# Kernel tuning notes

Hardware: AMD Instinct MI355X
Metric: run time of the kernel (lower is better)

Reference implementation:

```python
import jax, jax.numpy as jnp
import numpy as np

SEQ_LEN = 4096
D_IN = 1024
D_OUT = 1024


def setup_inputs() -> dict:
    key = jax.random.key(0)
    k_x, k_q, k_k, k_v = jax.random.split(key, 4)
    s = 1.0 / np.sqrt(D_IN)
    return {
        "x": jax.random.normal(k_x, (SEQ_LEN, D_IN), dtype=jnp.float32),
        "W_query": jax.random.normal(k_q, (D_IN, D_OUT), dtype=jnp.float32) * s,
        "W_key": jax.random.normal(k_k, (D_IN, D_OUT), dtype=jnp.float32) * s,
        "W_value": jax.random.normal(k_v, (D_IN, D_OUT), dtype=jnp.float32) * s,
    }


def reference(x, W_query, W_key, W_value):
    # QKV projections (Linear without bias): [S, d_out]
    q = x @ W_query
    k = x @ W_key
    v = x @ W_value
    # Full S x S score matrix, causal mask, scaled softmax
    scores = q @ k.T  # [S, S]
    seq_len = x.shape[0]
    causal = jnp.tril(jnp.ones((seq_len, seq_len), dtype=bool))
    scores = jnp.where(causal, scores, -jnp.inf)
    scale = 1.0 / jnp.sqrt(jnp.asarray(k.shape[-1], dtype=scores.dtype))
    attn = jax.nn.softmax(scores * scale, axis=-1)
    return attn @ v  # [S, d_out]
```

## Files before the change

### kernel.cpp

```cpp
#include <hip/hip_runtime.h>
#include <math.h>

#define SEQ 4096
#define DIM 1024

typedef unsigned short u16;
typedef __attribute__((ext_vector_type(8))) short short8;
typedef __attribute__((ext_vector_type(4))) float floatx4;
typedef __attribute__((ext_vector_type(4))) unsigned short us4;

__device__ __forceinline__ float bf2f(u16 u) {
    union { unsigned int i; float f; } c; c.i = ((unsigned int)u) << 16; return c.f;
}
__device__ __forceinline__ u16 f2bf(float f) {
    union { float f; unsigned int i; } c; c.f = f;
    return (u16)((c.i + 0x7fffu + ((c.i >> 16) & 1u)) >> 16);
}
__device__ __forceinline__ void gload_lds16(const u16* g, u16* l) {
    __builtin_amdgcn_global_load_lds((const __attribute__((address_space(1))) void*)g,
                                     (__attribute__((address_space(3))) void*)l, 16, 0, 0);
}

__global__ __launch_bounds__(256) void gemm_qkv(const u16* __restrict__ A,
                                                const u16* __restrict__ B,
                                                u16* __restrict__ QK,
                                                u16* __restrict__ VtOut) {
    const int row0 = blockIdx.x * 128;
    const int col0 = blockIdx.y * 128;

    __shared__ u16 As[3][4096];
    __shared__ u16 Bs[3][4096];

    const int tid  = threadIdx.x;
    const int wave = tid >> 6;
    const int lane = tid & 63;
    const int wm = wave & 1;
    const int wn = wave >> 1;

    const int s0 = wave * 128 + lane;
    const int s1 = s0 + 64;
    const int r0s = s0 >> 2, q0s = ((s0 & 3) ^ ((s0 >> 3) & 3)) * 8;
    const int r1s = s1 >> 2, q1s = ((s1 & 3) ^ ((s1 >> 3) & 3)) * 8;
    const u16* aP0 = A + (size_t)(row0 + r0s) * DIM + q0s;
    const u16* aP1 = A + (size_t)(row0 + r1s) * DIM + q1s;
    const u16* bP0 = B + (size_t)(col0 + r0s) * DIM + q0s;
    const u16* bP1 = B + (size_t)(col0 + r1s) * DIM + q1s;
    const int l0 = wave * 1024;

    floatx4 acc[4][4] = {};
    const int niter = DIM >> 5;
    const int frow = lane & 15;
    const int xq = (((lane >> 4) ^ ((frow >> 1) & 3))) * 8;

    gload_lds16(aP0, &As[0][l0]);
    gload_lds16(aP1, &As[0][l0 + 512]);
    gload_lds16(bP0, &Bs[0][l0]);
    gload_lds16(bP1, &Bs[0][l0 + 512]);
    aP0 += 32; aP1 += 32; bP0 += 32; bP1 += 32;
    gload_lds16(aP0, &As[1][l0]);
    gload_lds16(aP1, &As[1][l0 + 512]);
    gload_lds16(bP0, &Bs[1][l0]);
    gload_lds16(bP1, &Bs[1][l0 + 512]);
    aP0 += 32; aP1 += 32; bP0 += 32; bP1 += 32;

    auto compute_tile = [&](int c) {
        short8 af[4], bfr[4];
#pragma unroll
        for (int t = 0; t < 4; ++t) {
            af[t]  = *(const short8*)&As[c][(wm * 64 + t * 16 + frow) * 32 + xq];
            bfr[t] = *(const short8*)&Bs[c][(wn * 64 + t * 16 + frow) * 32 + xq];
        }
#pragma unroll
        for (int mt = 0; mt < 4; ++mt)
#pragma unroll
            for (int nt = 0; nt < 4; ++nt)
                acc[mt][nt] = __builtin_amdgcn_mfma_f32_16x16x32_bf16(
                    af[mt], bfr[nt], acc[mt][nt], 0, 0, 0);
    };

    int cur = 0, pre = 2;
    for (int it = 0; it < niter - 2; ++it) {
        asm volatile("s_waitcnt vmcnt(4)\n\ts_barrier" ::: "memory");
        short8 af[4], bfr[4];
#pragma unroll
        for (int t = 0; t < 4; ++t) {
            af[t]  = *(const short8*)&As[cur][(wm * 64 + t * 16 + frow) * 32 + xq];
            bfr[t] = *(const short8*)&Bs[cur][(wn * 64 + t * 16 + frow) * 32 + xq];
        }
        gload_lds16(aP0, &As[pre][l0]);
        gload_lds16(aP1, &As[pre][l0 + 512]);
        gload_lds16(bP0, &Bs[pre][l0]);
        gload_lds16(bP1, &Bs[pre][l0 + 512]);
        aP0 += 32; aP1 += 32; bP0 += 32; bP1 += 32;
#pragma unroll
        for (int mt = 0; mt < 4; ++mt)
#pragma unroll
            for (int nt = 0; nt < 4; ++nt)
                acc[mt][nt] = __builtin_amdgcn_mfma_f32_16x16x32_bf16(
                    af[mt], bfr[nt], acc[mt][nt], 0, 0, 0);
        cur = (cur == 2) ? 0 : cur + 1;
        pre = (pre == 2) ? 0 : pre + 1;
    }
    asm volatile("s_waitcnt vmcnt(4)\n\ts_barrier" ::: "memory");
    compute_tile(cur);
    cur = (cur == 2) ? 0 : cur + 1;
    asm volatile("s_waitcnt vmcnt(0)\n\ts_barrier" ::: "memory");
    compute_tile(cur);

    const int cr = (lane >> 4) * 4;
    const int cc = lane & 15;
    if (col0 >= 2048) {
#pragma unroll
        for (int mt = 0; mt < 4; ++mt)
#pragma unroll
            for (int nt = 0; nt < 4; ++nt) {
                const int row = row0 + wm * 64 + mt * 16 + cr;
                const int col = (col0 - 2048) + wn * 64 + nt * 16 + cc;
                us4 o = { f2bf(acc[mt][nt][0]), f2bf(acc[mt][nt][1]),
                          f2bf(acc[mt][nt][2]), f2bf(acc[mt][nt][3]) };
                *(us4*)&VtOut[(size_t)col * SEQ + row] = o;
            }
    } else {
        const float sc = (col0 < 1024) ? 0.03125f : 1.0f;
#pragma unroll
        for (int mt = 0; mt < 4; ++mt)
#pragma unroll
            for (int nt = 0; nt < 4; ++nt)
#pragma unroll
                for (int r = 0; r < 4; ++r) {
                    const int row = row0 + wm * 64 + mt * 16 + cr + r;
                    const int col = col0 + wn * 64 + nt * 16 + cc;
                    QK[(size_t)row * 2048 + col] = f2bf(acc[mt][nt][r] * sc);
                }
    }
}

template <int SCORES>
__global__ __launch_bounds__(512, 4) void gemm_att(const u16* __restrict__ A,
                                                   const u16* __restrict__ B,
                                                   void* __restrict__ Cv,
                                                   float* __restrict__ Lsum,
                                                   int lda, int ldb) {
    int row0, col0, kbeg = 0, kend;
    if (SCORES) {
        col0 = blockIdx.x * 128;
        row0 = blockIdx.y * 128;
        if (col0 > row0) return;
        kend = DIM;
    } else {
        const int u = blockIdx.x;
        col0 = blockIdx.y * 128;
        int r, c;
        if (u < 32)      { c = 0; r = u; }
        else if (u < 56) { c = 1; r = u - 24; }
        else if (u < 72) { c = 2; r = u - 40; }
        else             { c = 3; r = u - 48; }
        row0 = r * 128;
        kbeg = c << 10;
        kend = min(kbeg + 1024, row0 + 128);
    }

    __shared__ u16 As[3][4096];
    __shared__ u16 Bs[3][4096];

    const int tid  = threadIdx.x;
    const int wave = tid >> 6;
    const int lane = tid & 63;
    const int wm = wave & 1;
    const int wn = wave >> 1;

    const int sw = wave & 3;
    const int s0 = sw * 128 + lane;
    const int s1 = s0 + 64;
    const int r0s = s0 >> 2, q0s = ((s0 & 3) ^ ((s0 >> 3) & 3)) * 8;
    const int r1s = s1 >> 2, q1s = ((s1 & 3) ^ ((s1 >> 3) & 3)) * 8;
    const bool isA = wave < 4;
    const u16* p0 = isA ? A + (size_t)(row0 + r0s) * lda + kbeg + q0s
                        : B + (size_t)(col0 + r0s) * ldb + kbeg + q0s;
    const u16* p1 = isA ? A + (size_t)(row0 + r1s) * lda + kbeg + q1s
                        : B + (size_t)(col0 + r1s) * ldb + kbeg + q1s;
    const int o0 = s0 * 8;
    const int o1 = o0 + 512;

    floatx4 acc[4][2] = {};
    const int niter = (kend - kbeg) >> 5;
    const int frow = lane & 15;
    const int xq = (((lane >> 4) ^ ((frow >> 1) & 3))) * 8;

    {
        u16* d0 = isA ? &As[0][0] : &Bs[0][0];
        gload_lds16(p0, d0 + o0);
        gload_lds16(p1, d0 + o1);
        p0 += 32; p1 += 32;
        u16* d1 = isA ? &As[1][0] : &Bs[1][0];
        gload_lds16(p0, d1 + o0);
        gload_lds16(p1, d1 + o1);
        p0 += 32; p1 += 32;
    }

    auto compute_tile = [&](int c) {
        short8 af[4], bfr[2];
#pragma unroll
        for (int t = 0; t < 4; ++t)
            af[t] = *(const short8*)&As[c][(wm * 64 + t * 16 + frow) * 32 + xq];
#pragma unroll
        for (int t = 0; t < 2; ++t)
            bfr[t] = *(const short8*)&Bs[c][(wn * 32 + t * 16 + frow) * 32 + xq];
#pragma unroll
        for (int mt = 0; mt < 4; ++mt)
#pragma unroll
            for (int nt = 0; nt < 2; ++nt)
                acc[mt][nt] = __builtin_amdgcn_mfma_f32_16x16x32_bf16(
                    af[mt], bfr[nt], acc[mt][nt], 0, 0, 0);
    };

    int cur = 0, pre = 2;
    for (int it = 0; it < niter - 2; ++it) {
        asm volatile("s_waitcnt vmcnt(2)\n\ts_barrier" ::: "memory");
        short8 af[4], bfr[2];
#pragma unroll
        for (int t = 0; t < 4; ++t)
            af[t] = *(const short8*)&As[cur][(wm * 64 + t * 16 + frow) * 32 + xq];
#pragma unroll
        for (int t = 0; t < 2; ++t)
            bfr[t] = *(const short8*)&Bs[cur][(wn * 32 + t * 16 + frow) * 32 + xq];
        u16* dp = isA ? &As[pre][0] : &Bs[pre][0];
        gload_lds16(p0, dp + o0);
        gload_lds16(p1, dp + o1);
        p0 += 32; p1 += 32;
#pragma unroll
        for (int mt = 0; mt < 4; ++mt)
#pragma unroll
            for (int nt = 0; nt < 2; ++nt)
                acc[mt][nt] = __builtin_amdgcn_mfma_f32_16x16x32_bf16(
                    af[mt], bfr[nt], acc[mt][nt], 0, 0, 0);
        cur = (cur == 2) ? 0 : cur + 1;
        pre = (pre == 2) ? 0 : pre + 1;
    }
    asm volatile("s_waitcnt vmcnt(2)\n\ts_barrier" ::: "memory");
    compute_tile(cur);
    cur = (cur == 2) ? 0 : cur + 1;
    asm volatile("s_waitcnt vmcnt(0)\n\ts_barrier" ::: "memory");
    compute_tile(cur);

    const int cr = (lane >> 4) * 4;
    const int cc = lane & 15;
    if (SCORES) {
        u16* E = (u16*)Cv;
#pragma unroll
        for (int mt = 0; mt < 4; ++mt) {
#pragma unroll
            for (int r = 0; r < 4; ++r) {
                const int grow = row0 + wm * 64 + mt * 16 + cr + r;
                float rowsum = 0.f;
#pragma unroll
                for (int nt = 0; nt < 2; ++nt) {
                    const int gcol = col0 + wn * 32 + nt * 16 + cc;
                    const float e = (gcol <= grow) ? __expf(acc[mt][nt][r]) : 0.f;
                    rowsum += e;
                    E[(size_t)grow * SEQ + gcol] = f2bf(e);
                }
                rowsum += __shfl_xor(rowsum, 1);
                rowsum += __shfl_xor(rowsum, 2);
                rowsum += __shfl_xor(rowsum, 4);
                rowsum += __shfl_xor(rowsum, 8);
                if (cc == 0) atomicAdd(&Lsum[grow], rowsum);
            }
        }
    } else {
        float* O = (float*)Cv;
#pragma unroll
        for (int mt = 0; mt < 4; ++mt)
#pragma unroll
            for (int r = 0; r < 4; ++r) {
                const int grow = row0 + wm * 64 + mt * 16 + cr + r;
                const float invl = 1.0f / Lsum[grow];
#pragma unroll
                for (int nt = 0; nt < 2; ++nt) {
                    const int col = col0 + wn * 32 + nt * 16 + cc;
                    atomicAdd(&O[(size_t)grow * DIM + col], acc[mt][nt][r] * invl);
                }
            }
    }
}

__global__ __launch_bounds__(256) void prep(const float* __restrict__ x,
                                            const float* __restrict__ W0,
                                            const float* __restrict__ W1,
                                            const float* __restrict__ W2,
                                            u16* __restrict__ xb,
                                            u16* __restrict__ Wt,
                                            float* __restrict__ O,
                                            float* __restrict__ Lsum) {
    __shared__ float tile[32][33];
    const int b = blockIdx.x;
    const int tid = threadIdx.x;
    if (b < 4096) {
        const size_t i = ((size_t)b * 256 + tid) * 4;
        const float4 v = *(const float4*)(x + i);
        us4 o = { f2bf(v.x), f2bf(v.y), f2bf(v.z), f2bf(v.w) };
        *(us4*)(xb + i) = o;
    } else if (b < 7168) {
        const int t = b - 4096;
        const int z = t >> 10;
        const int idx = t & 1023;
        const float* W = (z == 0) ? W0 : (z == 1) ? W1 : W2;
        u16* out = Wt + (size_t)z * DIM * DIM;
        const int bx = (idx & 31) * 32;
        const int by = (idx >> 5) * 32;
        const int tx = tid & 31;
        const int ty = (tid >> 5) * 4;
#pragma unroll
        for (int r = 0; r < 4; ++r)
            tile[ty + r][tx] = W[(size_t)(by + ty + r) * DIM + bx + tx];
        __syncthreads();
#pragma unroll
        for (int r = 0; r < 4; ++r)
            out[(size_t)(bx + ty + r) * DIM + by + tx] = f2bf(tile[tx][ty + r]);
    } else {
        const int t = b - 7168;
        const size_t i = ((size_t)t * 256 + tid) * 4;
        *(float4*)(O + i) = make_float4(0.f, 0.f, 0.f, 0.f);
        if (t < 4) *(float4*)(Lsum + (size_t)(t * 256 + tid) * 4) =
            make_float4(0.f, 0.f, 0.f, 0.f);
    }
}

extern "C" void kernel_launch(void* const* d_in, const int* in_sizes, int n_in,
                              void* d_out, int out_size, void* d_ws, size_t ws_size,
                              hipStream_t stream) {
    const float* x  = (const float*)d_in[0];
    const float* Wq = (const float*)d_in[1];
    const float* Wk = (const float*)d_in[2];
    const float* Wv = (const float*)d_in[3];

    u16* xb   = (u16*)d_ws;
    u16* Wt   = xb + (size_t)SEQ * DIM;
    u16* QK   = Wt + (size_t)3072 * DIM;
    u16* Vt   = QK + (size_t)SEQ * 2048;
    u16* E    = Vt + (size_t)DIM * SEQ;
    float* Lsum = (float*)(E + (size_t)SEQ * SEQ);

    prep<<<8192, 256, 0, stream>>>(x, Wq, Wk, Wv, xb, Wt, (float*)d_out, Lsum);

    gemm_qkv<<<dim3(32, 24), 256, 0, stream>>>(xb, Wt, QK, Vt);

    gemm_att<1><<<dim3(32, 32), 512, 0, stream>>>(
        QK, QK + 1024, E, Lsum, 2048, 2048);

    gemm_att<0><<<dim3(80, 8), 512, 0, stream>>>(
        E, Vt, d_out, Lsum, SEQ, SEQ);
}
```

Before: 209.3 us.

## Restructure attention GEMMs to 4-wave blocks with 64-wide K tiles and triangular grid

The scores and PV kernels move from 512-thread blocks with a 32-wide K step and triple buffering to 256-thread blocks with a 64-wide K step and double buffering. Each wave now computes a 64x64 sub-tile with a 4x4 MFMA accumulator, which gives more data reuse per LDS read. The scores launch becomes a 1D triangular grid of 528 blocks, so no blocks are launched only to exit, and the PV grid swaps its x and y axes. The costs are a full vmcnt(0) wait every iteration, meaning less load/compute overlap, and more registers per wave.

```diff
diff --git a/kernel.cpp b/kernel.cpp
--- a/kernel.cpp
+++ b/kernel.cpp
@@ -136,20 +136,24 @@
 }
 
 template <int SCORES>
-__global__ __launch_bounds__(512, 4) void gemm_att(const u16* __restrict__ A,
-                                                   const u16* __restrict__ B,
-                                                   void* __restrict__ Cv,
-                                                   float* __restrict__ Lsum,
-                                                   int lda, int ldb) {
+__global__ __launch_bounds__(256) void gemm_att64(const u16* __restrict__ A,
+                                                  const u16* __restrict__ B,
+                                                  void* __restrict__ Cv,
+                                                  float* __restrict__ Lsum,
+                                                  int lda, int ldb) {
     int row0, col0, kbeg = 0, kend;
     if (SCORES) {
-        col0 = blockIdx.x * 128;
-        row0 = blockIdx.y * 128;
-        if (col0 > row0) return;
+        const int t = blockIdx.x;
+        int by = (int)((sqrtf(8.0f * t + 1.0f) - 1.0f) * 0.5f);
+        while ((by + 1) * (by + 2) / 2 <= t) ++by;
+        while (by * (by + 1) / 2 > t) --by;
+        const int bx = t - by * (by + 1) / 2;
+        row0 = by * 128;
+        col0 = bx * 128;
         kend = DIM;
     } else {
-        const int u = blockIdx.x;
-        col0 = blockIdx.y * 128;
+        col0 = blockIdx.x * 128;
+        const int u = blockIdx.y;
         int r, c;
         if (u < 32)      { c = 0; r = u; }
         else if (u < 56) { c = 1; r = u - 24; }
@@ -160,8 +164,8 @@
         kend = min(kbeg + 1024, row0 + 128);
     }
 
-    __shared__ u16 As[3][4096];
-    __shared__ u16 Bs[3][4096];
+    __shared__ u16 As[2][8192];
+    __shared__ u16 Bs[2][8192];
 
     const int tid  = threadIdx.x;
     const int wave = tid >> 6;
@@ -169,79 +173,64 @@
     const int wm = wave & 1;
     const int wn = wave >> 1;
 
-    const int sw = wave & 3;
-    const int s0 = sw * 128 + lane;
-    const int s1 = s0 + 64;
-    const int r0s = s0 >> 2, q0s = ((s0 & 3) ^ ((s0 >> 3) & 3)) * 8;
-    const int r1s = s1 >> 2, q1s = ((s1 & 3) ^ ((s1 >> 3) & 3)) * 8;
-    const bool isA = wave < 4;
-    const u16* p0 = isA ? A + (size_t)(row0 + r0s) * lda + kbeg + q0s
-                        : B + (size_t)(col0 + r0s) * ldb + kbeg + q0s;
-    const u16* p1 = isA ? A + (size_t)(row0 + r1s) * lda + kbeg + q1s
-                        : B + (size_t)(col0 + r1s) * ldb + kbeg + q1s;
-    const int o0 = s0 * 8;
-    const int o1 = o0 + 512;
-
-    floatx4 acc[4][2] = {};
-    const int niter = (kend - kbeg) >> 5;
+    const u16* aP[4];
+    const u16* bP[4];
+    int dOff[4];
+#pragma unroll
+    for (int j = 0; j < 4; ++j) {
+        const int s = wave * 256 + j * 64 + lane;
+        const int r = s >> 3;
+        const int q = (s & 7) ^ (r & 7);
+        aP[j] = A + (size_t)(row0 + r) * lda + kbeg + q * 8;
+        bP[j] = B + (size_t)(col0 + r) * ldb + kbeg + q * 8;
+        dOff[j] = s * 8;
+    }
+
+    floatx4 acc[4][4] = {};
+    const int niter = (kend - kbeg) >> 6;
     const int frow = lane & 15;
-    const int xq = (((lane >> 4) ^ ((frow >> 1) & 3))) * 8;
-
-    {
-        u16* d0 = isA ? &As[0][0] : &Bs[0][0];
-        gload_lds16(p0, d0 + o0);
-        gload_lds16(p1, d0 + o1);
-        p0 += 32; p1 += 32;
-        u16* d1 = isA ? &As[1][0] : &Bs[1][0];
-        gload_lds16(p0, d1 + o0);
-        gload_lds16(p1, d1 + o1);
-        p0 += 32; p1 += 32;
-    }
-
-    auto compute_tile = [&](int c) {
-        short8 af[4], bfr[2];
-#pragma unroll
-        for (int t = 0; t < 4; ++t)
-            af[t] = *(const short8*)&As[c][(wm * 64 + t * 16 + frow) * 32 + xq];
-#pragma unroll
-        for (int t = 0; t < 2; ++t)
-            bfr[t] = *(const short8*)&Bs[c][(wn * 32 + t * 16 + frow) * 32 + xq];
-#pragma unroll
-        for (int mt = 0; mt < 4; ++mt)
-#pragma unroll
-            for (int nt = 0; nt < 2; ++nt)
-                acc[mt][nt] = __builtin_amdgcn_mfma_f32_16x16x32_bf16(
-                    af[mt], bfr[nt], acc[mt][nt], 0, 0, 0);
-    };
-
-    int cur = 0, pre = 2;
-    for (int it = 0; it < niter - 2; ++it) {
-        asm volatile("s_waitcnt vmcnt(2)\n\ts_barrier" ::: "memory");
-        short8 af[4], bfr[2];
-#pragma unroll
-        for (int t = 0; t < 4; ++t)
-            af[t] = *(const short8*)&As[cur][(wm * 64 + t * 16 + frow) * 32 + xq];
-#pragma unroll
-        for (int t = 0; t < 2; ++t)
-            bfr[t] = *(const short8*)&Bs[cur][(wn * 32 + t * 16 + frow) * 32 + xq];
-        u16* dp = isA ? &As[pre][0] : &Bs[pre][0];
-        gload_lds16(p0, dp + o0);
-        gload_lds16(p1, dp + o1);
-        p0 += 32; p1 += 32;
-#pragma unroll
-        for (int mt = 0; mt < 4; ++mt)
-#pragma unroll
-            for (int nt = 0; nt < 2; ++nt)
-                acc[mt][nt] = __builtin_amdgcn_mfma_f32_16x16x32_bf16(
-                    af[mt], bfr[nt], acc[mt][nt], 0, 0, 0);
-        cur = (cur == 2) ? 0 : cur + 1;
-        pre = (pre == 2) ? 0 : pre + 1;
-    }
-    asm volatile("s_waitcnt vmcnt(2)\n\ts_barrier" ::: "memory");
-    compute_tile(cur);
-    cur = (cur == 2) ? 0 : cur + 1;
-    asm volatile("s_waitcnt vmcnt(0)\n\ts_barrier" ::: "memory");
-    compute_tile(cur);
+    const int grp  = lane >> 4;
+
+#pragma unroll
+    for (int j = 0; j < 4; ++j) {
+        gload_lds16(aP[j], &As[0][dOff[j]]);
+        gload_lds16(bP[j], &Bs[0][dOff[j]]);
+        aP[j] += 64; bP[j] += 64;
+    }
+
+    for (int it = 0; it < niter; ++it) {
+        asm volatile("s_waitcnt vmcnt(0)\n\ts_barrier" ::: "memory");
+        const int cur = it & 1;
+        short8 af[2][4], bfr[2][4];
+#pragma unroll
+        for (int ks = 0; ks < 2; ++ks)
+#pragma unroll
+            for (int t = 0; t < 4; ++t) {
+                const int ar = wm * 64 + t * 16 + frow;
+                const int ca = (ks * 4 + grp) ^ (ar & 7);
+                af[ks][t] = *(const short8*)&As[cur][ar * 64 + ca * 8];
+                const int br = wn * 64 + t * 16 + frow;
+                const int cb = (ks * 4 + grp) ^ (br & 7);
+                bfr[ks][t] = *(const short8*)&Bs[cur][br * 64 + cb * 8];
+            }
+        if (it + 1 < niter) {
+            const int nxt = cur ^ 1;
+#pragma unroll
+            for (int j = 0; j < 4; ++j) {
+                gload_lds16(aP[j], &As[nxt][dOff[j]]);
+                gload_lds16(bP[j], &Bs[nxt][dOff[j]]);
+                aP[j] += 64; bP[j] += 64;
+            }
+        }
+#pragma unroll
+        for (int ks = 0; ks < 2; ++ks)
+#pragma unroll
+            for (int mt = 0; mt < 4; ++mt)
+#pragma unroll
+                for (int nt = 0; nt < 4; ++nt)
+                    acc[mt][nt] = __builtin_amdgcn_mfma_f32_16x16x32_bf16(
+                        af[ks][mt], bfr[ks][nt], acc[mt][nt], 0, 0, 0);
+    }
 
     const int cr = (lane >> 4) * 4;
     const int cc = lane & 15;
@@ -254,8 +243,8 @@
                 const int grow = row0 + wm * 64 + mt * 16 + cr + r;
                 float rowsum = 0.f;
 #pragma unroll
-                for (int nt = 0; nt < 2; ++nt) {
-                    const int gcol = col0 + wn * 32 + nt * 16 + cc;
+                for (int nt = 0; nt < 4; ++nt) {
+                    const int gcol = col0 + wn * 64 + nt * 16 + cc;
                     const float e = (gcol <= grow) ? __expf(acc[mt][nt][r]) : 0.f;
                     rowsum += e;
                     E[(size_t)grow * SEQ + gcol] = f2bf(e);
@@ -276,8 +265,8 @@
                 const int grow = row0 + wm * 64 + mt * 16 + cr + r;
                 const float invl = 1.0f / Lsum[grow];
 #pragma unroll
-                for (int nt = 0; nt < 2; ++nt) {
-                    const int col = col0 + wn * 32 + nt * 16 + cc;
+                for (int nt = 0; nt < 4; ++nt) {
+                    const int col = col0 + wn * 64 + nt * 16 + cc;
                     atomicAdd(&O[(size_t)grow * DIM + col], acc[mt][nt][r] * invl);
                 }
             }
@@ -345,9 +334,7 @@
 
     gemm_qkv<<<dim3(32, 24), 256, 0, stream>>>(xb, Wt, QK, Vt);
 
-    gemm_att<1><<<dim3(32, 32), 512, 0, stream>>>(
-        QK, QK + 1024, E, Lsum, 2048, 2048);
-
-    gemm_att<0><<<dim3(80, 8), 512, 0, stream>>>(
-        E, Vt, d_out, Lsum, SEQ, SEQ);
-}
+    gemm_att64<1><<<528, 256, 0, stream>>>(QK, QK + 1024, E, Lsum, 2048, 2048);
+
+    gemm_att64<0><<<dim3(8, 80), 256, 0, stream>>>(E, Vt, d_out, Lsum, SEQ, SEQ);
+}
```

Result: no change. 206.0 us (-1.6%).
